# Performance work log

Hardware: AMD Instinct MI355X
Metric: run time of the kernel (lower is better)

Reference implementation:

```python
import jax, jax.numpy as jnp
import numpy as np
import math

FACTOR = 1  # init kwarg

def setup_inputs() -> dict:
    key = jax.random.key(0)
    k1, k2 = jax.random.split(key)
    B, H, C, L = 32, 8, 64, 1024
    values = jax.random.normal(k1, (B, H, C, L), dtype=jnp.float32)
    corr = jax.random.uniform(k2, (B, H, C, L), dtype=jnp.float32)
    return {"values": values, "corr": corr}

def reference(values, corr):
    # Faithful translation of Auto_attn.time_delay_training.
    B, H, C, L = values.shape
    top_k = int(FACTOR * math.log(L))  # static: depends only on L
    # mean over head then channel -> [B, L]
    mean_value = corr.mean(axis=(1, 2))
    # top-k delays shared across the batch (argmax of batch-mean correlation)
    _, index = jax.lax.top_k(mean_value.mean(axis=0), top_k)  # [top_k]
    # per-batch weights at the selected delays -> [B, top_k]
    weights = mean_value[:, index]
    tmp_corr = jax.nn.softmax(weights, axis=-1)  # [B, top_k]
    # roll(values, -index[i], axis=-1) == gather at (t + index[i]) mod L
    gather_idx = (jnp.arange(L)[None, :] + index[:, None]) % L  # [top_k, L]
    pattern = jnp.take(values, gather_idx, axis=-1)  # [B, H, C, top_k, L]
    # softmax-weighted aggregation over the top_k delays
    delays_agg = jnp.einsum('bhckl,bk->bhcl', pattern, tmp_corr)
    return delays_agg
```

## Files before the change

### kernel.cpp

```cpp
#include <hip/hip_runtime.h>
#include <math.h>

#define B 32
#define H 8
#define C 64
#define L 1024
#define HC (H * C)
#define K 6

#define SLICES 8
#define SLICE_L (L / SLICES)
#define GROUPS1 16
#define ROWS_PER_GROUP (HC / GROUPS1)

__global__ __launch_bounds__(512) void mean_value_kernel(
    const float* __restrict__ corr, float* __restrict__ mean_value) {
    __shared__ float sacc[GROUPS1 * SLICE_L];
    int blk = blockIdx.x;
    int b = blk / SLICES;
    int s = blk % SLICES;
    int t = threadIdx.x;
    int g = t >> 5;
    int j = t & 31;

    const float4* base =
        (const float4*)(corr + (size_t)b * HC * L + s * SLICE_L);
    float4 acc = make_float4(0.f, 0.f, 0.f, 0.f);
    #pragma unroll 8
    for (int i = 0; i < ROWS_PER_GROUP; ++i) {
        int r = g + GROUPS1 * i;
        float4 v = base[(size_t)r * (L / 4) + j];
        acc.x += v.x; acc.y += v.y; acc.z += v.z; acc.w += v.w;
    }
    ((float4*)sacc)[g * (SLICE_L / 4) + j] = acc;
    __syncthreads();

    if (t < SLICE_L) {
        float m = 0.f;
        #pragma unroll
        for (int g2 = 0; g2 < GROUPS1; ++g2) m += sacc[g2 * SLICE_L + t];
        mean_value[b * L + s * SLICE_L + t] = m * (1.0f / HC);
    }
}

__global__ __launch_bounds__(1024) void topk_softmax_kernel(
    const float* __restrict__ mean_value,
    float* __restrict__ tmp_corr,
    int* __restrict__ index_out) {
    __shared__ float wval[16];
    __shared__ int   widx[16];
    __shared__ int   sel[K];
    int t = threadIdx.x;
    int lane = t & 63;
    int wave = t >> 6;

    float s = 0.f;
    #pragma unroll
    for (int b = 0; b < B; ++b) s += mean_value[b * L + t];
    float cm = s * (1.0f / B);
    int   ci = t;

    for (int k = 0; k < K; ++k) {
        float v = cm; int i = ci;
        #pragma unroll
        for (int off = 32; off >= 1; off >>= 1) {
            float v2 = __shfl_xor(v, off, 64);
            int   i2 = __shfl_xor(i, off, 64);
            if (v2 > v || (v2 == v && i2 < i)) { v = v2; i = i2; }
        }
        if (lane == 0) { wval[wave] = v; widx[wave] = i; }
        __syncthreads();
        if (wave == 0) {
            float v3 = (lane < 16) ? wval[lane] : -3.0e38f;
            int   i3 = (lane < 16) ? widx[lane] : 0x7fffffff;
            #pragma unroll
            for (int off = 8; off >= 1; off >>= 1) {
                float v2 = __shfl_xor(v3, off, 64);
                int   i2 = __shfl_xor(i3, off, 64);
                if (v2 > v3 || (v2 == v3 && i2 < i3)) { v3 = v2; i3 = i2; }
            }
            if (lane == 0) sel[k] = i3;
        }
        __syncthreads();
        if (ci == sel[k]) cm = -3.0e38f;
    }

    if (t < K) index_out[t] = sel[t];
    if (t < B) {
        float w[K];
        float m = -3.0e38f;
        for (int k = 0; k < K; ++k) {
            w[k] = mean_value[t * L + sel[k]];
            m = fmaxf(m, w[k]);
        }
        float sum = 0.f;
        for (int k = 0; k < K; ++k) { w[k] = expf(w[k] - m); sum += w[k]; }
        float inv = 1.0f / sum;
        for (int k = 0; k < K; ++k) tmp_corr[t * K + k] = w[k] * inv;
    }
}

__global__ __launch_bounds__(256) void agg_kernel(
    const float* __restrict__ values,
    const float* __restrict__ tmp_corr,
    const int* __restrict__ index,
    float* __restrict__ out) {
    __shared__ float row[2 * L];
    __shared__ float ws[K];
    __shared__ int   is[K];
    int blk = blockIdx.x;
    int b = blk / HC;
    int tid = threadIdx.x;

    float4 v = ((const float4*)(values + (size_t)blk * L))[tid];
    ((float4*)row)[tid] = v;
    ((float4*)row)[tid + 256] = v;
    if (tid < K) { ws[tid] = tmp_corr[b * K + tid]; is[tid] = index[tid]; }
    __syncthreads();

    float w[K]; int d[K];
    #pragma unroll
    for (int k = 0; k < K; ++k) { w[k] = ws[k]; d[k] = is[k]; }

    int l0 = tid * 4;
    float4 acc = make_float4(0.f, 0.f, 0.f, 0.f);
    #pragma unroll
    for (int k = 0; k < K; ++k) {
        const float* p = row + l0 + d[k];
        acc.x += w[k] * p[0];
        acc.y += w[k] * p[1];
        acc.z += w[k] * p[2];
        acc.w += w[k] * p[3];
    }
    ((float4*)(out + (size_t)blk * L))[tid] = acc;
}

extern "C" void kernel_launch(void* const* d_in, const int* in_sizes, int n_in,
                              void* d_out, int out_size, void* d_ws, size_t ws_size,
                              hipStream_t stream) {
    const float* values = (const float*)d_in[0];
    const float* corr   = (const float*)d_in[1];
    float* out = (float*)d_out;

    float* mean_value = (float*)d_ws;
    float* tmp_corr   = mean_value + (size_t)B * L;
    int*   index      = (int*)(tmp_corr + B * K);

    mean_value_kernel<<<B * SLICES, 512, 0, stream>>>(corr, mean_value);
    topk_softmax_kernel<<<1, 1024, 0, stream>>>(mean_value, tmp_corr, index);
    agg_kernel<<<B * H * C, 256, 0, stream>>>(values, tmp_corr, index, out);
}
```

Measured before the change: 182.0 us.

## Rework top-k as single-wave scan, widen mean reduction, stride agg accesses

```diff
diff --git a/kernel.cpp b/kernel.cpp
--- a/kernel.cpp
+++ b/kernel.cpp
@@ -10,10 +10,10 @@
 
 #define SLICES 8
 #define SLICE_L (L / SLICES)
-#define GROUPS1 16
+#define GROUPS1 32
 #define ROWS_PER_GROUP (HC / GROUPS1)
 
-__global__ __launch_bounds__(512) void mean_value_kernel(
+__global__ __launch_bounds__(1024) void mean_value_kernel(
     const float* __restrict__ corr, float* __restrict__ mean_value) {
     __shared__ float sacc[GROUPS1 * SLICE_L];
     int blk = blockIdx.x;
@@ -43,60 +43,70 @@
     }
 }
 
-__global__ __launch_bounds__(1024) void topk_softmax_kernel(
+__global__ __launch_bounds__(256) void topk_softmax_kernel(
     const float* __restrict__ mean_value,
     float* __restrict__ tmp_corr,
     int* __restrict__ index_out) {
-    __shared__ float wval[16];
-    __shared__ int   widx[16];
-    __shared__ int   sel[K];
+    __shared__ float cm[L];
     int t = threadIdx.x;
-    int lane = t & 63;
-    int wave = t >> 6;
 
-    float s = 0.f;
+    float4 s4 = make_float4(0.f, 0.f, 0.f, 0.f);
     #pragma unroll
-    for (int b = 0; b < B; ++b) s += mean_value[b * L + t];
-    float cm = s * (1.0f / B);
-    int   ci = t;
+    for (int b = 0; b < B; ++b) {
+        float4 v = ((const float4*)(mean_value + (size_t)b * L))[t];
+        s4.x += v.x; s4.y += v.y; s4.z += v.z; s4.w += v.w;
+    }
+    float4 c4 = make_float4(s4.x * (1.0f / B), s4.y * (1.0f / B),
+                            s4.z * (1.0f / B), s4.w * (1.0f / B));
+    ((float4*)cm)[t] = c4;
+    __syncthreads();
 
-    for (int k = 0; k < K; ++k) {
-        float v = cm; int i = ci;
+    if (t < 64) {
+        float val[16];
         #pragma unroll
-        for (int off = 32; off >= 1; off >>= 1) {
-            float v2 = __shfl_xor(v, off, 64);
-            int   i2 = __shfl_xor(i, off, 64);
-            if (v2 > v || (v2 == v && i2 < i)) { v = v2; i = i2; }
+        for (int q = 0; q < 4; ++q) {
+            float4 v = ((float4*)cm)[t * 4 + q];
+            val[q * 4 + 0] = v.x; val[q * 4 + 1] = v.y;
+            val[q * 4 + 2] = v.z; val[q * 4 + 3] = v.w;
         }
-        if (lane == 0) { wval[wave] = v; widx[wave] = i; }
-        __syncthreads();
-        if (wave == 0) {
-            float v3 = (lane < 16) ? wval[lane] : -3.0e38f;
-            int   i3 = (lane < 16) ? widx[lane] : 0x7fffffff;
+        int sel[K];
+        #pragma unroll
+        for (int k = 0; k < K; ++k) {
+            float best = -3.0e38f; int bi = 0x7fffffff;
             #pragma unroll
-            for (int off = 8; off >= 1; off >>= 1) {
-                float v2 = __shfl_xor(v3, off, 64);
-                int   i2 = __shfl_xor(i3, off, 64);
-                if (v2 > v3 || (v2 == v3 && i2 < i3)) { v3 = v2; i3 = i2; }
+            for (int m = 0; m < 16; ++m) {
+                if (val[m] > best) { best = val[m]; bi = t * 16 + m; }
             }
-            if (lane == 0) sel[k] = i3;
+            #pragma unroll
+            for (int off = 32; off >= 1; off >>= 1) {
+                float v2 = __shfl_xor(best, off, 64);
+                int   i2 = __shfl_xor(bi, off, 64);
+                if (v2 > best || (v2 == best && i2 < bi)) { best = v2; bi = i2; }
+            }
+            sel[k] = bi;
+            #pragma unroll
+            for (int m = 0; m < 16; ++m)
+                if (t * 16 + m == bi) val[m] = -3.0e38f;
         }
-        __syncthreads();
-        if (ci == sel[k]) cm = -3.0e38f;
-    }
-
-    if (t < K) index_out[t] = sel[t];
-    if (t < B) {
-        float w[K];
-        float m = -3.0e38f;
-        for (int k = 0; k < K; ++k) {
-            w[k] = mean_value[t * L + sel[k]];
-            m = fmaxf(m, w[k]);
+        if (t == 0) {
+            #pragma unroll
+            for (int k = 0; k < K; ++k) index_out[k] = sel[k];
         }
-        float sum = 0.f;
-        for (int k = 0; k < K; ++k) { w[k] = expf(w[k] - m); sum += w[k]; }
-        float inv = 1.0f / sum;
-        for (int k = 0; k < K; ++k) tmp_corr[t * K + k] = w[k] * inv;
+        if (t < B) {
+            float w[K];
+            float m = -3.0e38f;
+            #pragma unroll
+            for (int k = 0; k < K; ++k) {
+                w[k] = mean_value[t * L + sel[k]];
+                m = fmaxf(m, w[k]);
+            }
+            float sum = 0.f;
+            #pragma unroll
+            for (int k = 0; k < K; ++k) { w[k] = expf(w[k] - m); sum += w[k]; }
+            float inv = 1.0f / sum;
+            #pragma unroll
+            for (int k = 0; k < K; ++k) tmp_corr[t * K + k] = w[k] * inv;
+        }
     }
 }
 
@@ -122,17 +132,20 @@
     #pragma unroll
     for (int k = 0; k < K; ++k) { w[k] = ws[k]; d[k] = is[k]; }
 
-    int l0 = tid * 4;
-    float4 acc = make_float4(0.f, 0.f, 0.f, 0.f);
+    float a0 = 0.f, a1 = 0.f, a2 = 0.f, a3 = 0.f;
     #pragma unroll
     for (int k = 0; k < K; ++k) {
-        const float* p = row + l0 + d[k];
-        acc.x += w[k] * p[0];
-        acc.y += w[k] * p[1];
-        acc.z += w[k] * p[2];
-        acc.w += w[k] * p[3];
+        const float* p = row + tid + d[k];
+        a0 += w[k] * p[0];
+        a1 += w[k] * p[256];
+        a2 += w[k] * p[512];
+        a3 += w[k] * p[768];
     }
-    ((float4*)(out + (size_t)blk * L))[tid] = acc;
+    float* orow = out + (size_t)blk * L;
+    orow[tid]       = a0;
+    orow[tid + 256] = a1;
+    orow[tid + 512] = a2;
+    orow[tid + 768] = a3;
 }
 
 extern "C" void kernel_launch(void* const* d_in, const int* in_sizes, int n_in,
@@ -146,7 +159,7 @@
     float* tmp_corr   = mean_value + (size_t)B * L;
     int*   index      = (int*)(tmp_corr + B * K);
 
-    mean_value_kernel<<<B * SLICES, 512, 0, stream>>>(corr, mean_value);
-    topk_softmax_kernel<<<1, 1024, 0, stream>>>(mean_value, tmp_corr, index);
+    mean_value_kernel<<<B * SLICES, 1024, 0, stream>>>(corr, mean_value);
+    topk_softmax_kernel<<<1, 256, 0, stream>>>(mean_value, tmp_corr, index);
     agg_kernel<<<B * H * C, 256, 0, stream>>>(values, tmp_corr, index, out);
 }
```

Result: faster. 175.1 us (-3.8%).
